# Optimization experiments

Hardware: AMD Instinct MI355X
Metric: run time of the kernel (lower is better)

## Reference

```python
import jax, jax.numpy as jnp
import numpy as np

THRESHOLD = 0.5
N_SEG = 5
NEG_INF = -1e30
EPS = 1e-12  # F.normalize eps


def setup_inputs() -> dict:
    key = jax.random.key(0)
    kx, kl = jax.random.split(key)
    B, D, L = 4096, 512, 80
    x = jax.random.normal(kx, (B, D), dtype=jnp.float32)
    labels = jax.random.randint(kl, (B, L), 0, 2, dtype=jnp.int32)
    return {"x": x, "labels": labels}


def reference(x, labels):
    B = x.shape[0]
    labels_f = labels.astype(jnp.float32)
    # pairwise Jaccard over multi-hot labels
    intersection = labels_f @ labels_f.T                      # [B, B]
    counts = labels_f.sum(axis=1, keepdims=True)              # [B, 1]
    union = counts + counts.T - intersection
    jaccard = intersection / union                            # [B, B]
    # cosine similarity (F.normalize with eps clamp)
    norm = jnp.maximum(jnp.linalg.norm(x, axis=1, keepdims=True), EPS)
    nx = x / norm
    sim = nx @ nx.T                                           # [B, B]
    # --- sample positive (uniform among jaccard > threshold), fixed key ---
    pos_mask = jaccard > THRESHOLD
    valid_mask = jnp.any(pos_mask, axis=1)                    # [B]
    logits = jnp.where(pos_mask, 0.0, NEG_INF)
    sampled = jax.random.categorical(jax.random.key(42), logits, axis=-1)
    pos_samples = jnp.where(valid_mask, sampled, 0)           # invalid rows -> 0
    # --- top-k negatives: jaccard strictly below the positive's jaccard ---
    pos_sim_j = jaccard[jnp.arange(B), pos_samples]           # [B]
    neg_mask = jaccard < pos_sim_j[:, None]
    neg_sims = jnp.where(neg_mask, jaccard, -jnp.inf)
    _, neg_samples = jax.lax.top_k(neg_sims, N_SEG)           # [B, N_SEG]
    # --- contrastive loss on cosine sims at sampled indices ---
    rel_pos = sim[jnp.arange(B), pos_samples]                 # [B]
    rel_neg = jnp.take_along_axis(sim, neg_samples, axis=1)   # [B, N_SEG]
    exp_pos = jnp.exp(rel_pos)
    sum_exp_neg = jnp.exp(rel_neg).sum(axis=1)
    loss = -jnp.log(exp_pos / (exp_pos + sum_exp_neg))
    vm = valid_mask.astype(x.dtype)
    return (loss * vm).sum() / vm.sum()
```

## Files before the change

kernel.cpp:

```cpp
#include <hip/hip_runtime.h>
#include <stdint.h>

#define B_ROWS 4096
#define DIMS   512
#define NLAB   80
#define HALF_ROWS 2048
#define HCNT   8388608u
#define CHUNK  1024
#define SEGCAP 512u
#define NBLK   2048

typedef unsigned long long u64;

__device__ __forceinline__ uint32_t rotl32(uint32_t x, uint32_t d) {
    return (x << d) | (x >> (32u - d));
}

__device__ __forceinline__ void tf2x32_key42(uint32_t c0, uint32_t c1,
                                             uint32_t& o0, uint32_t& o1) {
    const uint32_t ks0 = 0u;
    const uint32_t ks1 = 42u;
    const uint32_t ks2 = 0x1BD11BDAu ^ 0u ^ 42u;
    uint32_t x0 = c0 + ks0;
    uint32_t x1 = c1 + ks1;
#define TF_RND(r) { x0 += x1; x1 = rotl32(x1, (r)); x1 ^= x0; }
    TF_RND(13u) TF_RND(15u) TF_RND(26u) TF_RND(6u)
    x0 += ks1; x1 += ks2 + 1u;
    TF_RND(17u) TF_RND(29u) TF_RND(16u) TF_RND(24u)
    x0 += ks2; x1 += ks0 + 2u;
    TF_RND(13u) TF_RND(15u) TF_RND(26u) TF_RND(6u)
    x0 += ks0; x1 += ks1 + 3u;
    TF_RND(17u) TF_RND(29u) TF_RND(16u) TF_RND(24u)
    x0 += ks1; x1 += ks2 + 4u;
    TF_RND(13u) TF_RND(15u) TF_RND(26u) TF_RND(6u)
    x0 += ks2; x1 += ks0 + 5u;
#undef TF_RND
    o0 = x0; o1 = x1;
}

__device__ __forceinline__ u64 shflx64(u64 v, int m) {
    uint32_t lo = __shfl_xor((uint32_t)(v & 0xFFFFFFFFull), m, 64);
    uint32_t hi = __shfl_xor((uint32_t)(v >> 32), m, 64);
    return ((u64)hi << 32) | (u64)lo;
}

__device__ __forceinline__ uint32_t umx(uint32_t a, uint32_t b) { return a > b ? a : b; }
__device__ __forceinline__ uint32_t umn(uint32_t a, uint32_t b) { return a < b ? a : b; }

__device__ __forceinline__ uint32_t mbcnt64(u64 m) {
    uint32_t c = __builtin_amdgcn_mbcnt_lo((uint32_t)m, 0u);
    return __builtin_amdgcn_mbcnt_hi((uint32_t)(m >> 32), c);
}

__device__ __forceinline__ void ins5_u32(uint32_t* t, uint32_t k) {
    t[4] = umx(t[4], k);
    uint32_t hi, lo;
    hi = umx(t[3], t[4]); lo = umn(t[3], t[4]); t[3] = hi; t[4] = lo;
    hi = umx(t[2], t[3]); lo = umn(t[2], t[3]); t[2] = hi; t[3] = lo;
    hi = umx(t[1], t[2]); lo = umn(t[1], t[2]); t[1] = hi; t[2] = lo;
    hi = umx(t[0], t[1]); lo = umn(t[0], t[1]); t[0] = hi; t[1] = lo;
}

__device__ __forceinline__ void merge5_u32(uint32_t* A, const uint32_t* Bv) {
    uint32_t a0=A[0],a1=A[1],a2=A[2],a3=A[3],a4=A[4];
    uint32_t b0=Bv[0],b1=Bv[1],b2=Bv[2],b3=Bv[3],b4=Bv[4];
    uint32_t m0 = umx(a0, b0);
    uint32_t m1 = umx(umx(a1, b1), umn(a0, b0));
    uint32_t m2 = umx(umx(a2, b2), umx(umn(a0, b1), umn(a1, b0)));
    uint32_t m3 = umx(umx(a3, b3), umx(umx(umn(a0, b2), umn(a1, b1)), umn(a2, b0)));
    uint32_t m4 = umx(umx(a4, b4), umx(umx(umn(a0, b3), umn(a1, b2)),
                                       umx(umn(a2, b1), umn(a3, b0))));
    A[0]=m0; A[1]=m1; A[2]=m2; A[3]=m3; A[4]=m4;
}

__device__ __forceinline__ void wave_top5_2(uint32_t* ta, uint32_t* tb,
                                            uint32_t* fa, uint32_t* fb) {
#pragma unroll
    for (int k = 0; k < 5; ++k) {
        uint32_t ma = ta[0], mb = tb[0];
#pragma unroll
        for (int s = 1; s < 64; s <<= 1) {
            ma = umx(ma, __shfl_xor(ma, s, 64));
            mb = umx(mb, __shfl_xor(mb, s, 64));
        }
        fa[k] = ma; fb[k] = mb;
        if (ta[0] == ma) { ta[0]=ta[1]; ta[1]=ta[2]; ta[2]=ta[3]; ta[3]=ta[4]; ta[4]=0u; }
        if (tb[0] == mb) { tb[0]=tb[1]; tb[1]=tb[2]; tb[2]=tb[3]; tb[3]=tb[4]; tb[4]=0u; }
    }
}

__device__ __forceinline__ uint32_t jkey19(uint32_t it, uint32_t u) {
    const uint32_t n = it << 19;
    float f = (float)it * __builtin_amdgcn_rcpf((float)u) * 524288.0f;
    uint32_t ak = (uint32_t)f;
    int r = (int)(n - ak * u);
    if (r < 0) { ak--; r += (int)u; }
    if (r >= (int)u) ak++;
    return ak + 1u;
}


__global__ __launch_bounds__(256) void prep_kernel(const float* __restrict__ x,
                                                   const int* __restrict__ labels,
                                                   uint4* __restrict__ pk,
                                                   float* __restrict__ norms) {
    const int tid = threadIdx.x;
    const int lane = tid & 63;
    const int row = blockIdx.x * 4 + (tid >> 6);
    const int* lr = labels + (size_t)row * NLAB;
    const int la = lr[lane];
    const int lb = (lane < 16) ? lr[64 + lane] : 0;
    const u64 b0 = __ballot(la != 0);
    const u64 b1 = __ballot(lb != 0);
    const uint32_t w2 = (uint32_t)b1 & 0xFFFFu;
    const uint32_t cnt = (uint32_t)__popcll(b0) + (uint32_t)__popc(w2);
    if (lane == 0) pk[row] = make_uint4((uint32_t)b0, (uint32_t)(b0 >> 32), w2, cnt);
    const float* xr = x + (size_t)row * DIMS;
    float ss = 0.f;
#pragma unroll
    for (int u = 0; u < 8; ++u) { float v = xr[lane + 64 * u]; ss += v * v; }
#pragma unroll
    for (int m = 1; m < 64; m <<= 1) ss += __shfl_xor(ss, m, 64);
    if (lane == 0) norms[row] = fmaxf(sqrtf(ss), 1e-12f);
}

__global__ __launch_bounds__(256) void fused_kernel(const float* __restrict__ x,
                                                    const uint4* __restrict__ pk,
                                                    const float* __restrict__ norms,
                                                    float2* __restrict__ blockPart) {
    __shared__ uint32_t segL[2][4][SEGCAP];
    __shared__ uint32_t cntL[2][4];
    __shared__ u64      gpart[2][4];
    __shared__ uint32_t keysL[2][4][5];
    __shared__ uint32_t posL[2], pjkeyL[2], validL[2];
    __shared__ uint32_t tgL[2][6];
    __shared__ float    simsL[2][6];
    __shared__ float    lossW[2], cntW2[2];

    const int tid = threadIdx.x;
    const int lane = tid & 63;
    const int sub  = tid >> 6;
    const int pr   = (int)blockIdx.x;
    const int r0 = pr, r1 = pr + HALF_ROWS;
    const uint4 P0 = pk[r0], P1 = pk[r1];
    const uint32_t cw0 = P0.w, cw1 = P1.w;
    const int jbase = sub * CHUNK;

    uint32_t cnt0 = 0u, cnt1 = 0u;
#pragma unroll 8
    for (int jb = 0; jb < CHUNK; jb += 64) {
        const int j = jbase + jb + lane;
        const uint4 pj = pk[j];
        const uint32_t cj = pj.w;
        const uint32_t it0 = (uint32_t)(__popc(P0.x & pj.x) + __popc(P0.y & pj.y) + __popc(P0.z & pj.z));
        const uint32_t u0  = cw0 + cj - it0;
        const uint32_t it1 = (uint32_t)(__popc(P1.x & pj.x) + __popc(P1.y & pj.y) + __popc(P1.z & pj.z));
        const uint32_t u1  = cw1 + cj - it1;
        const bool b0 = __umul24(it0, 20u) >= __umul24(u0, 9u);
        const bool b1 = __umul24(it1, 20u) >= __umul24(u1, 9u);
        const u64 bal0 = __ballot(b0);
        const u64 bal1 = __ballot(b1);
        if (b0) {
            const uint32_t off = cnt0 + mbcnt64(bal0);
            if (off < SEGCAP) segL[0][sub][off] = (it0 << 20) | (u0 << 12) | (uint32_t)j;
        }
        cnt0 += (uint32_t)__popcll(bal0);
        if (b1) {
            const uint32_t off = cnt1 + mbcnt64(bal1);
            if (off < SEGCAP) segL[1][sub][off] = (it1 << 20) | (u1 << 12) | (uint32_t)j;
        }
        cnt1 += (uint32_t)__popcll(bal1);
    }
    if (lane == 0) { cntL[0][sub] = cnt0; cntL[1][sub] = cnt1; }
    __syncthreads();

    const uint32_t base23 = (uint32_t)pr * (uint32_t)B_ROWS;
#pragma unroll
    for (int h = 0; h < 2; ++h) {
        const int n = (int)umn(cntL[h][sub], SEGCAP);
        u64 gb = 0ull;
        for (int e = lane; e < n; e += 64) {
            const uint32_t ent = segL[h][sub][e];
            const uint32_t u  = (ent >> 12) & 0xFFu;
            const uint32_t it = ent >> 20;
            if ((it << 1) > u) {
                const uint32_t j = ent & 0xFFFu;
                uint32_t o0, o1;
                tf2x32_key42(base23 + j, base23 + j + HCNT, o0, o1);
                const uint32_t o = h ? o1 : o0;
                const u64 key = ((u64)(o >> 9) << 41) | ((u64)((~j) & 0xFFFu) << 29) | (u64)jkey19(it, u);
                if (key > gb) gb = key;
            }
        }
#pragma unroll
        for (int m = 1; m < 64; m <<= 1) {
            const u64 o = shflx64(gb, m);
            if (o > gb) gb = o;
        }
        if (lane == 0) gpart[h][sub] = gb;
    }
    __syncthreads();

    if (sub < 2 && lane == 0) {
        const int h = sub;
        u64 g = gpart[h][0];
        if (gpart[h][1] > g) g = gpart[h][1];
        if (gpart[h][2] > g) g = gpart[h][2];
        if (gpart[h][3] > g) g = gpart[h][3];
        const bool valid = g != 0ull;
        validL[h] = valid ? 1u : 0u;
        posL[h]   = valid ? ((~(uint32_t)(g >> 29)) & 0xFFFu) : 0u;
        pjkeyL[h] = (uint32_t)(g & 0xFFFFFu);
    }
    __syncthreads();

    {
        const uint32_t pj0 = pjkeyL[0], pj1 = pjkeyL[1];
        const int n0 = (int)umn(cntL[0][sub], SEGCAP);
        const int n1 = (int)umn(cntL[1][sub], SEGCAP);
        uint32_t t0[5] = {0u,0u,0u,0u,0u}, t1[5] = {0u,0u,0u,0u,0u};
        uint32_t thr0 = 0u, thr1 = 0u;
        for (int e = lane; e < n0; e += 64) {
            const uint32_t ent = segL[0][sub][e];
            const uint32_t u  = (ent >> 12) & 0xFFu;
            const uint32_t it = ent >> 20;
            if ((it << 19) >= thr0 * u) {
                const uint32_t j  = ent & 0xFFFu;
                const uint32_t k19 = jkey19(it, u);
                const uint32_t key = (k19 < pj0) ? ((k19 << 12) | ((~j) & 0xFFFu)) : 0u;
                if (key > t0[4]) {
                    ins5_u32(t0, key);
                    thr0 = umx(t0[4] >> 12, 1u) - 1u;
                }
            }
        }
        for (int e = lane; e < n1; e += 64) {
            const uint32_t ent = segL[1][sub][e];
            const uint32_t u  = (ent >> 12) & 0xFFu;
            const uint32_t it = ent >> 20;
            if ((it << 19) >= thr1 * u) {
                const uint32_t j  = ent & 0xFFFu;
                const uint32_t k19 = jkey19(it, u);
                const uint32_t key = (k19 < pj1) ? ((k19 << 12) | ((~j) & 0xFFFu)) : 0u;
                if (key > t1[4]) {
                    ins5_u32(t1, key);
                    thr1 = umx(t1[4] >> 12, 1u) - 1u;
                }
            }
        }
        uint32_t f0[5], f1[5];
        wave_top5_2(t0, t1, f0, f1);
        if (lane == 0) {
#pragma unroll
            for (int k = 0; k < 5; ++k) { keysL[0][sub][k] = f0[k]; keysL[1][sub][k] = f1[k]; }
        }
    }
    __syncthreads();

    if (sub < 2 && lane == 0) {
        const int h = sub;
        uint32_t f[5];
#pragma unroll
        for (int k = 0; k < 5; ++k) f[k] = keysL[h][0][k];
#pragma unroll
        for (int s = 1; s < 4; ++s) merge5_u32(f, keysL[h][s]);
        tgL[h][0] = posL[h];
#pragma unroll
        for (int k = 0; k < 5; ++k) tgL[h][k + 1] = (~f[k]) & 0xFFFu;
    }
    __syncthreads();

#pragma unroll
    for (int k = 0; k < 3; ++k) {
        const int d = sub + 4 * k;
        const int h = (d >= 6) ? 1 : 0;
        const int q = d - 6 * h;
        const int row = h ? r1 : r0;
        const int tgt = (int)tgL[h][q];
        const float* pa = x + (size_t)row * DIMS;
        const float* pb = x + (size_t)tgt * DIMS;
        float s = 0.f;
#pragma unroll
        for (int u = 0; u < 8; ++u) s += pa[lane + 64 * u] * pb[lane + 64 * u];
#pragma unroll
        for (int m = 1; m < 64; m <<= 1) s += __shfl_xor(s, m, 64);
        if (lane == 0) simsL[h][q] = s;
    }
    __syncthreads();

    if (sub < 2 && lane == 0) {
        const int h = sub;
        float loss = 0.f, cnt = 0.f;
        if (validL[h]) {
            const int row = h ? r1 : r0;
            const float nr = norms[row];
            const float sp = simsL[h][0] / (nr * norms[tgL[h][0]]);
            float sen = 0.f;
#pragma unroll
            for (int q = 1; q < 6; ++q) sen += expf(simsL[h][q] / (nr * norms[tgL[h][q]]));
            const float ep = expf(sp);
            loss = -logf(ep / (ep + sen));
            cnt = 1.f;
        }
        lossW[h] = loss; cntW2[h] = cnt;
    }
    __syncthreads();
    if (tid == 0) blockPart[pr] = make_float2(lossW[0] + lossW[1], cntW2[0] + cntW2[1]);
}

__global__ __launch_bounds__(256) void final_kernel(const float2* __restrict__ blockPart,
                                                    float* __restrict__ out) {
    __shared__ float rl[4], rc[4];
    const int tid = threadIdx.x;
    const int lane = tid & 63;
    const int w = tid >> 6;
    float sl = 0.f, sc = 0.f;
#pragma unroll
    for (int k = 0; k < 8; ++k) {
        const float2 p = blockPart[tid + 256 * k];
        sl += p.x; sc += p.y;
    }
#pragma unroll
    for (int m = 1; m < 64; m <<= 1) {
        sl += __shfl_xor(sl, m, 64);
        sc += __shfl_xor(sc, m, 64);
    }
    if (lane == 0) { rl[w] = sl; rc[w] = sc; }
    __syncthreads();
    if (tid == 0) out[0] = (rl[0] + rl[1] + rl[2] + rl[3]) / (rc[0] + rc[1] + rc[2] + rc[3]);
}

extern "C" void kernel_launch(void* const* d_in, const int* in_sizes, int n_in,
                              void* d_out, int out_size, void* d_ws, size_t ws_size,
                              hipStream_t stream) {
    const float* x      = (const float*)d_in[0];
    const int*   labels = (const int*)d_in[1];
    float* out = (float*)d_out;

    char* ws = (char*)d_ws;
    uint4*  pk    = (uint4*)ws;
    float*  norms = (float*)(ws + 65536);
    float2* bPart = (float2*)(ws + 65536 + 16384);

    hipLaunchKernelGGL(prep_kernel,  dim3(1024), dim3(256), 0, stream, x, labels, pk, norms);
    hipLaunchKernelGGL(fused_kernel, dim3(NBLK), dim3(256), 0, stream, x, pk, norms, bPart);
    hipLaunchKernelGGL(final_kernel, dim3(1),    dim3(256), 0, stream, bPart, out);
}
```

Measured before the change: 88.74 us.

## Pair rows by label-count rank to balance per-block work

Each block now builds a histogram of label counts, prefix-sums it, and pairs the row of rank pr with the row of rank 4095-pr instead of rows pr and pr+2048. The aim is to balance the candidate-positive and RNG workload across blocks, since rows with few labels produce many Jaccard matches. The cost is that every block re-reads all 4096 packed label words to build the histogram and again to locate its rows by linear scan, adding shared atomics and extra syncs.

```diff
diff --git a/kernel.cpp b/kernel.cpp
--- a/kernel.cpp
+++ b/kernel.cpp
@@ -136,13 +136,66 @@
     __shared__ uint32_t tgL[2][6];
     __shared__ float    simsL[2][6];
     __shared__ float    lossW[2], cntW2[2];
+    __shared__ uint32_t hist4[4][81];
+    __shared__ uint32_t pfx[82];
+    __shared__ uint32_t rowsL[2];
 
     const int tid = threadIdx.x;
     const int lane = tid & 63;
     const int sub  = tid >> 6;
     const int pr   = (int)blockIdx.x;
-    const int r0 = pr, r1 = pr + HALF_ROWS;
-    const uint4 P0 = pk[r0], P1 = pk[r1];
+
+    if (tid < 81) { hist4[0][tid] = 0u; hist4[1][tid] = 0u; hist4[2][tid] = 0u; hist4[3][tid] = 0u; }
+    __syncthreads();
+#pragma unroll
+    for (int k = 0; k < 16; ++k) {
+        const uint32_t c = pk[tid + 256 * k].w;
+        atomicAdd(&hist4[sub][c], 1u);
+    }
+    __syncthreads();
+    if (sub == 0) {
+        const uint32_t v = hist4[0][lane] + hist4[1][lane] + hist4[2][lane] + hist4[3][lane];
+        uint32_t s = v;
+#pragma unroll
+        for (int d = 1; d < 64; d <<= 1) { const uint32_t t = __shfl_up(s, d, 64); if (lane >= d) s += t; }
+        pfx[lane] = s - v;
+        const uint32_t tot64 = __shfl(s, 63, 64);
+        uint32_t v2 = 0u;
+        if (lane < 17) v2 = hist4[0][64 + lane] + hist4[1][64 + lane] + hist4[2][64 + lane] + hist4[3][64 + lane];
+        uint32_t s2 = v2;
+#pragma unroll
+        for (int d = 1; d < 32; d <<= 1) { const uint32_t t = __shfl_up(s2, d, 64); if (lane >= d) s2 += t; }
+        if (lane < 17) pfx[64 + lane] = tot64 + s2 - v2;
+        if (lane == 16) pfx[81] = tot64 + s2;
+    }
+    __syncthreads();
+    if (sub < 2) {
+        const uint32_t R = sub ? (uint32_t)(4095 - pr) : (uint32_t)pr;
+        uint32_t c = (pfx[lane + 1] <= R) ? 1u : 0u;
+        if (lane < 17 && pfx[lane + 65] <= R) c += 1u;
+#pragma unroll
+        for (int m = 1; m < 64; m <<= 1) c += __shfl_xor(c, m, 64);
+        const uint32_t b = c;
+        uint32_t need = R - pfx[b];
+        uint32_t row = 0u;
+        for (int base = 0; base < B_ROWS; base += 64) {
+            const uint32_t cw = pk[base + lane].w;
+            const u64 m = __ballot(cw == b);
+            const uint32_t cc = (uint32_t)__popcll(m);
+            if (need < cc) {
+                const bool ok = (((m >> lane) & 1ull) != 0ull) && (mbcnt64(m) == need);
+                const u64 sel = __ballot(ok);
+                row = (uint32_t)base + (uint32_t)__builtin_ctzll(sel);
+                break;
+            }
+            need -= cc;
+        }
+        if (lane == 0) rowsL[sub] = row;
+    }
+    __syncthreads();
+    const int rA = (int)rowsL[0], rB = (int)rowsL[1];
+
+    const uint4 P0 = pk[rA], P1 = pk[rB];
     const uint32_t cw0 = P0.w, cw1 = P1.w;
     const int jbase = sub * CHUNK;
 
@@ -174,9 +227,11 @@
     if (lane == 0) { cntL[0][sub] = cnt0; cntL[1][sub] = cnt1; }
     __syncthreads();
 
-    const uint32_t base23 = (uint32_t)pr * (uint32_t)B_ROWS;
 #pragma unroll
     for (int h = 0; h < 2; ++h) {
+        const int rowH = h ? rB : rA;
+        const uint32_t baseH = ((uint32_t)rowH & 2047u) << 12;
+        const bool oselH = rowH >= 2048;
         const int n = (int)umn(cntL[h][sub], SEGCAP);
         u64 gb = 0ull;
         for (int e = lane; e < n; e += 64) {
@@ -186,8 +241,8 @@
             if ((it << 1) > u) {
                 const uint32_t j = ent & 0xFFFu;
                 uint32_t o0, o1;
-                tf2x32_key42(base23 + j, base23 + j + HCNT, o0, o1);
-                const uint32_t o = h ? o1 : o0;
+                tf2x32_key42(baseH + j, baseH + j + HCNT, o0, o1);
+                const uint32_t o = oselH ? o1 : o0;
                 const u64 key = ((u64)(o >> 9) << 41) | ((u64)((~j) & 0xFFFu) << 29) | (u64)jkey19(it, u);
                 if (key > gb) gb = key;
             }
@@ -275,7 +330,7 @@
         const int d = sub + 4 * k;
         const int h = (d >= 6) ? 1 : 0;
         const int q = d - 6 * h;
-        const int row = h ? r1 : r0;
+        const int row = h ? rB : rA;
         const int tgt = (int)tgL[h][q];
         const float* pa = x + (size_t)row * DIMS;
         const float* pb = x + (size_t)tgt * DIMS;
@@ -292,7 +347,7 @@
         const int h = sub;
         float loss = 0.f, cnt = 0.f;
         if (validL[h]) {
-            const int row = h ? r1 : r0;
+            const int row = h ? rB : rA;
             const float nr = norms[row];
             const float sp = simsL[h][0] / (nr * norms[tgL[h][0]]);
             float sen = 0.f;
```

Result: slower. 106.6 us (+20.1%).
